# Kernel tuning notes

Hardware: AMD Instinct MI355X
Metric: run time of the kernel (lower is better)

Reference implementation:

```python
import jax, jax.numpy as jnp
import numpy as np
from jax import lax

N, C_IN, H, W = 32, 128, 64, 64
C_OUT, KH, KW = 256, 3, 3
C_DIM = 64


def setup_inputs() -> dict:
    key = jax.random.key(0)
    k1, k2, k3, k4, k5 = jax.random.split(key, 5)
    return {
        "x": jax.random.normal(k1, (N, C_IN, H, W), dtype=jnp.float32),
        "c": jax.random.normal(k2, (N, C_DIM), dtype=jnp.float32),
        "weight": jax.random.normal(k3, (C_OUT, C_IN, KH, KW), dtype=jnp.float32),
        "c_weight": jax.random.normal(k4, (C_OUT, C_DIM), dtype=jnp.float32),
        "bias": jax.random.normal(k5, (C_OUT,), dtype=jnp.float32),
    }


def reference(x, c, weight, c_weight, bias):
    # Equivalent to the module's unfold + matmul path (groups=1, dilation=1,
    # zero padding=1, stride=1): a direct conv fused with the spatially
    # invariant context bias c @ c_weight^T and the channel bias.
    out = lax.conv_general_dilated(
        x, weight,
        window_strides=(1, 1),
        padding=((1, 1), (1, 1)),
        dimension_numbers=("NCHW", "OIHW", "NCHW"),
    )  # (N, C_out, H, W)
    ctx = jnp.einsum("nd,od->no", c, c_weight)  # (N, C_out), same at every spatial loc
    return out + ctx[:, :, None, None] + bias[None, :, None, None]
```

## Files before the change

kernel.cpp:

```cpp
#include <hip/hip_runtime.h>
#include <hip/hip_bf16.h>


#define NN   32
#define CIN  128
#define HH   64
#define WW   64
#define COUT 256
#define CDIM 64
#define HP   66
#define WP   66

#define XP_BYTES  ((size_t)NN*HP*WP*CIN*2)
#define WT_BYTES  ((size_t)9*COUT*CIN*2)
#define CTX_BYTES ((size_t)NN*COUT*4)
#define WS_NEEDED (XP_BYTES + WT_BYTES + CTX_BYTES)

typedef __attribute__((ext_vector_type(8))) short short8;
typedef __attribute__((ext_vector_type(4))) float float4v;

__device__ __forceinline__ void async16(const void* g, void* l) {
    __builtin_amdgcn_global_load_lds(
        (const __attribute__((address_space(1))) unsigned int*)g,
        (__attribute__((address_space(3))) unsigned int*)l, 16, 0, 0);
}

__global__ __launch_bounds__(256) void prep_x(const float* __restrict__ x,
                                              __hip_bfloat16* __restrict__ xP) {
    __shared__ float tile[CIN][65];
    int n = blockIdx.x >> 6;
    int h = blockIdx.x & 63;
    int t = threadIdx.x;
    const float* xb = x + (size_t)n * CIN * HH * WW + (size_t)h * WW;

    int lane16 = t & 15, rgrp = t >> 4;
    #pragma unroll
    for (int i = 0; i < 8; ++i) {
        int ci = rgrp + i * 16;
        float4v v = *(const float4v*)(xb + (size_t)ci * (HH * WW) + lane16 * 4);
        int w0 = lane16 * 4;
        tile[ci][w0]     = v.x;
        tile[ci][w0 + 1] = v.y;
        tile[ci][w0 + 2] = v.z;
        tile[ci][w0 + 3] = v.w;
    }
    __syncthreads();

    int oct = t & 3, w = t >> 2;
    __hip_bfloat16* db = xP + (((size_t)n * HP + (h + 1)) * WP + (w + 1)) * CIN;
    #pragma unroll
    for (int p = 0; p < 4; ++p) {
        int ci0 = p * 32 + oct * 8;
        union { short8 v; __hip_bfloat16 b[8]; } u;
        #pragma unroll
        for (int j = 0; j < 8; ++j)
            u.b[j] = __float2bfloat16(tile[ci0 + j][w]);
        *(short8*)(db + ci0) = u.v;
    }
}

__global__ __launch_bounds__(256) void prep_w(const float* __restrict__ wgt,
                                              __hip_bfloat16* __restrict__ wT) {
    int idx = blockIdx.x * 256 + threadIdx.x;
    int ci  = idx & 127;
    int co  = (idx >> 7) & 255;
    int tap = idx >> 15;
    wT[idx] = __float2bfloat16(wgt[((size_t)co * CIN + ci) * 9 + tap]);
}

__global__ __launch_bounds__(256) void prep_ctx(const float* __restrict__ c,
                                                const float* __restrict__ cw,
                                                const float* __restrict__ bias,
                                                float* __restrict__ ctx) {
    int idx = blockIdx.x * 256 + threadIdx.x;
    int co = idx & 255, n = idx >> 8;
    float a = bias[co];
    #pragma unroll 8
    for (int d = 0; d < CDIM; ++d) a += c[n * CDIM + d] * cw[co * CDIM + d];
    ctx[idx] = a;
}

__global__ __launch_bounds__(256) void conv_mfma(
    const __hip_bfloat16* __restrict__ xP,
    const __hip_bfloat16* __restrict__ wT,
    const float* __restrict__ ctx,
    float* __restrict__ out)
{
    __shared__ __align__(16) short A_s[4096];
    __shared__ __align__(16) short B_s[4096];

    int bid = blockIdx.x;
    int nt  = bid & 1;
    int mt  = bid >> 1;
    int n   = mt >> 5;
    int h0  = (mt & 31) << 1;

    int tid = threadIdx.x;
    int lane = tid & 63, wv = tid >> 6;
    int m0 = (wv & 1) * 64, n0 = (wv >> 1) * 64;

    int prow = wv * 32 + (lane >> 2);
    int pdst = (lane & 3) * 8;
    int qsrc = ((lane & 3) ^ ((lane >> 3) & 3)) * 8;
    int pc = (((lane >> 4) ^ (((lane & 15) >> 1) & 3))) * 8;

    float4v acc[4][4] = {};

    for (int kh = 0; kh < 3; ++kh)
    for (int kw = 0; kw < 3; ++kw) {
        int tap = kh * 3 + kw;
        for (int kb = 0; kb < 4; ++kb) {
            __syncthreads();
            #pragma unroll
            for (int i = 0; i < 2; ++i) {
                int p  = prow + i * 16;
                int hh = h0 + (p >> 6) + kh;
                int ww = (p & 63) + kw;
                const __hip_bfloat16* asrc =
                    xP + (((size_t)n * HP + hh) * WP + ww) * CIN + kb * 32 + qsrc;
                async16(asrc, &A_s[p * 32 + pdst]);
                const __hip_bfloat16* bsrc =
                    wT + ((size_t)tap * COUT + nt * 128 + p) * CIN + kb * 32 + qsrc;
                async16(bsrc, &B_s[p * 32 + pdst]);
            }
            __syncthreads();

            short8 aF[4], bF[4];
            #pragma unroll
            for (int mi = 0; mi < 4; ++mi)
                aF[mi] = *(const short8*)&A_s[(m0 + mi * 16 + (lane & 15)) * 32 + pc];
            #pragma unroll
            for (int ni = 0; ni < 4; ++ni)
                bF[ni] = *(const short8*)&B_s[(n0 + ni * 16 + (lane & 15)) * 32 + pc];
            #pragma unroll
            for (int mi = 0; mi < 4; ++mi)
                #pragma unroll
                for (int ni = 0; ni < 4; ++ni)
                    acc[mi][ni] = __builtin_amdgcn_mfma_f32_16x16x32_bf16(
                        aF[mi], bF[ni], acc[mi][ni], 0, 0, 0);
        }
    }

    #pragma unroll
    for (int ni = 0; ni < 4; ++ni) {
        int co = nt * 128 + n0 + ni * 16 + (lane & 15);
        float cv = ctx[n * COUT + co];
        #pragma unroll
        for (int mi = 0; mi < 4; ++mi) {
            int rp = m0 + mi * 16 + (lane >> 4) * 4;
            int hh = h0 + (rp >> 6);
            int ww = rp & 63;
            float4v v = acc[mi][ni] + cv;
            *(float4v*)&out[(((size_t)n * COUT + co) * HH + hh) * WW + ww] = v;
        }
    }
}

__global__ __launch_bounds__(256) void contextual_conv_f32(
    const float* __restrict__ x, const float* __restrict__ c,
    const float* __restrict__ wgt, const float* __restrict__ cw,
    const float* __restrict__ bias, float* __restrict__ out)
{
    int idx = blockIdx.x * 256 + threadIdx.x;
    int w = idx & 63, h = (idx >> 6) & 63, cb = (idx >> 12) & 63, n = idx >> 18;
    float acc[4];
    #pragma unroll
    for (int j = 0; j < 4; ++j) acc[j] = bias[cb + j * 64];
    const float* cp = c + n * CDIM;
    for (int d = 0; d < CDIM; ++d) {
        float cv = cp[d];
        #pragma unroll
        for (int j = 0; j < 4; ++j) acc[j] += cv * cw[(cb + j * 64) * CDIM + d];
    }
    const float* xn = x + (size_t)n * (CIN * HH * WW);
    for (int ci = 0; ci < CIN; ++ci) {
        const float* xc = xn + ci * (HH * WW);
        float wv[4][9];
        #pragma unroll
        for (int j = 0; j < 4; ++j) {
            const float* wp = wgt + ((cb + j * 64) * CIN + ci) * 9;
            #pragma unroll
            for (int k = 0; k < 9; ++k) wv[j][k] = wp[k];
        }
        #pragma unroll
        for (int kh = 0; kh < 3; ++kh) {
            int hh = h + kh - 1;
            if (hh < 0 || hh >= HH) continue;
            const float* xr = xc + hh * WW;
            #pragma unroll
            for (int kw = 0; kw < 3; ++kw) {
                int ww = w + kw - 1;
                if (ww < 0 || ww >= WW) continue;
                float xv = xr[ww];
                #pragma unroll
                for (int j = 0; j < 4; ++j) acc[j] += xv * wv[j][kh * 3 + kw];
            }
        }
    }
    size_t obase = (size_t)n * (COUT * HH * WW) + (size_t)h * WW + w;
    #pragma unroll
    for (int j = 0; j < 4; ++j)
        out[obase + (size_t)(cb + j * 64) * (HH * WW)] = acc[j];
}

extern "C" void kernel_launch(void* const* d_in, const int* in_sizes, int n_in,
                              void* d_out, int out_size, void* d_ws, size_t ws_size,
                              hipStream_t stream) {
    const float* x    = (const float*)d_in[0];
    const float* c    = (const float*)d_in[1];
    const float* wgt  = (const float*)d_in[2];
    const float* cw   = (const float*)d_in[3];
    const float* bias = (const float*)d_in[4];
    float* out = (float*)d_out;

    if (ws_size < WS_NEEDED) {
        const int total_threads = NN * 64 * HH * WW;
        contextual_conv_f32<<<total_threads / 256, 256, 0, stream>>>(x, c, wgt, cw, bias, out);
        return;
    }

    char* ws = (char*)d_ws;
    __hip_bfloat16* xP = (__hip_bfloat16*)ws;
    __hip_bfloat16* wT = (__hip_bfloat16*)(ws + XP_BYTES);
    float*          cx = (float*)(ws + XP_BYTES + WT_BYTES);

    hipMemsetAsync(ws, 0, XP_BYTES, stream);
    prep_x  <<<NN * HH, 256, 0, stream>>>(x, xP);
    prep_w  <<<(9 * COUT * CIN) / 256, 256, 0, stream>>>(wgt, wT);
    prep_ctx<<<(NN * COUT) / 256, 256, 0, stream>>>(c, cw, bias, cx);
    conv_mfma<<<2048, 256, 0, stream>>>(xP, wT, cx, out);
}
```

Measured before the change: 285.7 us.

## Zero only halo, merge weight/ctx prep, widen conv K-step to 64

```diff
diff --git a/kernel.cpp b/kernel.cpp
--- a/kernel.cpp
+++ b/kernel.cpp
@@ -25,6 +25,19 @@
         (__attribute__((address_space(3))) unsigned int*)l, 16, 0, 0);
 }
 
+__global__ __launch_bounds__(256) void zero_halo(__hip_bfloat16* __restrict__ xP) {
+    int g = blockIdx.x * 256 + threadIdx.x;
+    int n   = g / 4160;
+    int rem = g - n * 4160;
+    int pi  = rem >> 4;
+    int oct = rem & 15;
+    int hh, ww;
+    if (pi < 132) { hh = (pi >= 66) ? 65 : 0; ww = pi % 66; }
+    else { int p2 = pi - 132; ww = (p2 >= 64) ? 65 : 0; hh = 1 + (p2 & 63); }
+    short8 z = {};
+    *(short8*)(xP + (((size_t)n * HP + hh) * WP + ww) * CIN + oct * 8) = z;
+}
+
 __global__ __launch_bounds__(256) void prep_x(const float* __restrict__ x,
                                               __hip_bfloat16* __restrict__ xP) {
     __shared__ float tile[CIN][65];
@@ -59,25 +72,27 @@
     }
 }
 
-__global__ __launch_bounds__(256) void prep_w(const float* __restrict__ wgt,
-                                              __hip_bfloat16* __restrict__ wT) {
-    int idx = blockIdx.x * 256 + threadIdx.x;
-    int ci  = idx & 127;
-    int co  = (idx >> 7) & 255;
-    int tap = idx >> 15;
-    wT[idx] = __float2bfloat16(wgt[((size_t)co * CIN + ci) * 9 + tap]);
-}
-
-__global__ __launch_bounds__(256) void prep_ctx(const float* __restrict__ c,
-                                                const float* __restrict__ cw,
-                                                const float* __restrict__ bias,
-                                                float* __restrict__ ctx) {
-    int idx = blockIdx.x * 256 + threadIdx.x;
-    int co = idx & 255, n = idx >> 8;
-    float a = bias[co];
-    #pragma unroll 8
-    for (int d = 0; d < CDIM; ++d) a += c[n * CDIM + d] * cw[co * CDIM + d];
-    ctx[idx] = a;
+__global__ __launch_bounds__(256) void prep_wc(const float* __restrict__ wgt,
+                                               const float* __restrict__ c,
+                                               const float* __restrict__ cw,
+                                               const float* __restrict__ bias,
+                                               __hip_bfloat16* __restrict__ wT,
+                                               float* __restrict__ ctx) {
+    int bid = blockIdx.x;
+    if (bid < 1152) {
+        int idx = bid * 256 + threadIdx.x;
+        int ci  = idx & 127;
+        int co  = (idx >> 7) & 255;
+        int tap = idx >> 15;
+        wT[idx] = __float2bfloat16(wgt[((size_t)co * CIN + ci) * 9 + tap]);
+    } else {
+        int idx = (bid - 1152) * 256 + threadIdx.x;
+        int co = idx & 255, n = idx >> 8;
+        float a = bias[co];
+        #pragma unroll 8
+        for (int d = 0; d < CDIM; ++d) a += c[n * CDIM + d] * cw[co * CDIM + d];
+        ctx[idx] = a;
+    }
 }
 
 __global__ __launch_bounds__(256) void conv_mfma(
@@ -86,8 +101,8 @@
     const float* __restrict__ ctx,
     float* __restrict__ out)
 {
-    __shared__ __align__(16) short A_s[4096];
-    __shared__ __align__(16) short B_s[4096];
+    __shared__ __align__(16) short A_s[8192];
+    __shared__ __align__(16) short B_s[8192];
 
     int bid = blockIdx.x;
     int nt  = bid & 1;
@@ -99,45 +114,52 @@
     int lane = tid & 63, wv = tid >> 6;
     int m0 = (wv & 1) * 64, n0 = (wv >> 1) * 64;
 
-    int prow = wv * 32 + (lane >> 2);
-    int pdst = (lane & 3) * 8;
-    int qsrc = ((lane & 3) ^ ((lane >> 3) & 3)) * 8;
-    int pc = (((lane >> 4) ^ (((lane & 15) >> 1) & 3))) * 8;
+    int p0   = wv * 8 + (lane >> 3);
+    int q8   = ((lane & 7) ^ (lane >> 3)) * 8;
+    int dst0 = wv * 512 + lane * 8;
+
+    int cofs0 = ((0 * 4 + (lane >> 4)) ^ (lane & 7)) * 8;
+    int cofs1 = ((1 * 4 + (lane >> 4)) ^ (lane & 7)) * 8;
 
     float4v acc[4][4] = {};
 
     for (int kh = 0; kh < 3; ++kh)
     for (int kw = 0; kw < 3; ++kw) {
         int tap = kh * 3 + kw;
-        for (int kb = 0; kb < 4; ++kb) {
+        #pragma unroll
+        for (int kb = 0; kb < 2; ++kb) {
             __syncthreads();
             #pragma unroll
-            for (int i = 0; i < 2; ++i) {
-                int p  = prow + i * 16;
+            for (int i = 0; i < 4; ++i) {
+                int p  = p0 + i * 32;
                 int hh = h0 + (p >> 6) + kh;
                 int ww = (p & 63) + kw;
                 const __hip_bfloat16* asrc =
-                    xP + (((size_t)n * HP + hh) * WP + ww) * CIN + kb * 32 + qsrc;
-                async16(asrc, &A_s[p * 32 + pdst]);
+                    xP + (((size_t)n * HP + hh) * WP + ww) * CIN + kb * 64 + q8;
+                async16(asrc, &A_s[i * 2048 + dst0]);
                 const __hip_bfloat16* bsrc =
-                    wT + ((size_t)tap * COUT + nt * 128 + p) * CIN + kb * 32 + qsrc;
-                async16(bsrc, &B_s[p * 32 + pdst]);
+                    wT + ((size_t)tap * COUT + nt * 128 + p) * CIN + kb * 64 + q8;
+                async16(bsrc, &B_s[i * 2048 + dst0]);
             }
             __syncthreads();
 
-            short8 aF[4], bF[4];
-            #pragma unroll
-            for (int mi = 0; mi < 4; ++mi)
-                aF[mi] = *(const short8*)&A_s[(m0 + mi * 16 + (lane & 15)) * 32 + pc];
-            #pragma unroll
-            for (int ni = 0; ni < 4; ++ni)
-                bF[ni] = *(const short8*)&B_s[(n0 + ni * 16 + (lane & 15)) * 32 + pc];
-            #pragma unroll
-            for (int mi = 0; mi < 4; ++mi)
+            #pragma unroll
+            for (int kk = 0; kk < 2; ++kk) {
+                int cofs = kk ? cofs1 : cofs0;
+                short8 aF[4], bF[4];
+                #pragma unroll
+                for (int mi = 0; mi < 4; ++mi)
+                    aF[mi] = *(const short8*)&A_s[(m0 + mi * 16 + (lane & 15)) * 64 + cofs];
                 #pragma unroll
                 for (int ni = 0; ni < 4; ++ni)
-                    acc[mi][ni] = __builtin_amdgcn_mfma_f32_16x16x32_bf16(
-                        aF[mi], bF[ni], acc[mi][ni], 0, 0, 0);
+                    bF[ni] = *(const short8*)&B_s[(n0 + ni * 16 + (lane & 15)) * 64 + cofs];
+                #pragma unroll
+                for (int mi = 0; mi < 4; ++mi)
+                    #pragma unroll
+                    for (int ni = 0; ni < 4; ++ni)
+                        acc[mi][ni] = __builtin_amdgcn_mfma_f32_16x16x32_bf16(
+                            aF[mi], bF[ni], acc[mi][ni], 0, 0, 0);
+            }
         }
     }
 
@@ -224,9 +246,8 @@
     __hip_bfloat16* wT = (__hip_bfloat16*)(ws + XP_BYTES);
     float*          cx = (float*)(ws + XP_BYTES + WT_BYTES);
 
-    hipMemsetAsync(ws, 0, XP_BYTES, stream);
+    zero_halo<<<520, 256, 0, stream>>>(xP);
     prep_x  <<<NN * HH, 256, 0, stream>>>(x, xP);
-    prep_w  <<<(9 * COUT * CIN) / 256, 256, 0, stream>>>(wgt, wT);
-    prep_ctx<<<(NN * COUT) / 256, 256, 0, stream>>>(c, cw, bias, cx);
+    prep_wc <<<1184, 256, 0, stream>>>(wgt, c, cw, bias, wT, cx);
     conv_mfma<<<2048, 256, 0, stream>>>(xP, wT, cx, out);
 }
```

After: 268.0 us. 1.07x faster.
